# Performance work log

Measured on AMD Instinct MI355X. Metric: run time of the kernel, lower is better.

Reference implementation:

```python
import jax, jax.numpy as jnp
import numpy as np

D_MODEL = 1024
SCALE = 1.0 / np.sqrt(D_MODEL)


def setup_inputs() -> dict:
    key = jax.random.key(0)
    ks = jax.random.split(key, 9)
    B, S, D = 4, 2048, D_MODEL
    std = 1.0 / np.sqrt(D)
    x = jax.random.normal(ks[0], (B, S, D), dtype=jnp.float32)
    # nn.Linear weights: [out, in]; we store transposed [in, out] for x @ W
    Wq = jax.random.uniform(ks[1], (D, D), jnp.float32, -std, std)
    bq = jax.random.uniform(ks[2], (D,), jnp.float32, -std, std)
    Wk = jax.random.uniform(ks[3], (D, D), jnp.float32, -std, std)
    bk = jax.random.uniform(ks[4], (D,), jnp.float32, -std, std)
    Wv = jax.random.uniform(ks[5], (D, D), jnp.float32, -std, std)
    bv = jax.random.uniform(ks[6], (D,), jnp.float32, -std, std)
    Wo = jax.random.uniform(ks[7], (D, D), jnp.float32, -std, std)
    bo = jax.random.uniform(ks[8], (D,), jnp.float32, -std, std)
    return {"x": x, "Wq": Wq, "bq": bq, "Wk": Wk, "bk": bk,
            "Wv": Wv, "bv": bv, "Wo": Wo, "bo": bo}


def reference(x, Wq, bq, Wk, bk, Wv, bv, Wo, bo):
    q = x @ Wq + bq                      # [B,S,D]
    k = x @ Wk + bk
    v = x @ Wv + bv
    scores = jnp.einsum('bsd,btd->bst', q, k) * SCALE  # [B,S,S]
    weights = jax.nn.softmax(scores, axis=-1)
    out = jnp.einsum('bst,btd->bsd', weights, v)       # [B,S,D]
    return out @ Wo + bo
```

## Files before the change

### kernel.cpp

```cpp
#include <hip/hip_runtime.h>
#include <hip/hip_bf16.h>
#include <cstdint>

typedef __bf16 bf16x8 __attribute__((ext_vector_type(8)));
typedef float f32x4 __attribute__((ext_vector_type(4)));

__device__ __forceinline__ float bf2f(unsigned short u) {
  union { unsigned int i; float f; } x; x.i = ((unsigned int)u) << 16; return x.f;
}
__device__ __forceinline__ unsigned short f2bf(float f) {
  __hip_bfloat16 h = __float2bfloat16(f);
  return __builtin_bit_cast(unsigned short, h);
}

__device__ __forceinline__ void gload_lds16(const void* g, void* l) {
  auto gp = reinterpret_cast<__attribute__((address_space(1))) char*>(
      reinterpret_cast<uintptr_t>(g));
  auto lp = reinterpret_cast<__attribute__((address_space(3))) char*>(
      reinterpret_cast<uintptr_t>(l));
  __builtin_amdgcn_global_load_lds(gp, lp, 16, 0, 0);
}

__device__ __forceinline__ void xcd_swz(int& bx, int& by, int& bz) {
  const int gx = gridDim.x, gy = gridDim.y;
  const int n = gx * gy * (int)gridDim.z;
  int lin = blockIdx.x + gx * (blockIdx.y + gy * blockIdx.z);
  lin = (lin & 7) * (n >> 3) + (lin >> 3);
  bx = lin % gx; lin /= gx;
  by = lin % gy; bz = lin / gy;
}

__global__ __launch_bounds__(256) void cvt_f32_to_bf16(
    const float* __restrict__ in, unsigned short* __restrict__ out, long n4) {
  long i = (long)blockIdx.x * 256 + threadIdx.x;
  if (i >= n4) return;
  const float4 v = reinterpret_cast<const float4*>(in)[i];
  ushort4 o;
  o.x = f2bf(v.x); o.y = f2bf(v.y); o.z = f2bf(v.z); o.w = f2bf(v.w);
  reinterpret_cast<ushort4*>(out)[i] = o;
}

__global__ void transpose_w4(const float* __restrict__ w0,
                             const float* __restrict__ w1,
                             const float* __restrict__ w2,
                             const float* __restrict__ w3,
                             const float* __restrict__ b0,
                             const float* __restrict__ b1,
                             const float* __restrict__ b2,
                             unsigned short* __restrict__ out,
                             float* __restrict__ bqkv) {
  const int z = blockIdx.z;
  const float* in = (z == 0) ? w0 : (z == 1) ? w1 : (z == 2) ? w2 : w3;
  out += (size_t)z * 1024 * 1024;
  if (z < 3 && blockIdx.x == 0 && blockIdx.y == 0) {
    const float* src = (z == 0) ? b0 : (z == 1) ? b1 : b2;
    const int i = threadIdx.y * 32 + threadIdx.x;
    bqkv[z * 1024 + i] = src[i];
  }
  __shared__ float tile[32][33];
  const int c0 = blockIdx.x * 32, r0 = blockIdx.y * 32;
  tile[threadIdx.y][threadIdx.x] =
      in[(size_t)(r0 + threadIdx.y) * 1024 + c0 + threadIdx.x];
  __syncthreads();
  out[(size_t)(c0 + threadIdx.y) * 1024 + r0 + threadIdx.x] =
      f2bf(tile[threadIdx.x][threadIdx.y]);
}

template <typename OutT, bool HAS_BIAS, bool VSPLIT, bool EXPOUT, bool DIVSUM>
__global__ __launch_bounds__(256, 4) void gemm_hi(
    const unsigned short* __restrict__ A,
    const unsigned short* __restrict__ Bt,
    OutT* __restrict__ C,
    const float* __restrict__ bias,
    unsigned short* __restrict__ vt,
    int K, int lda, int ldb, int ldc, float scale,
    long sA, long sB, long sC) {
  int bx, by, bz;
  xcd_swz(bx, by, bz);
  A  += (long)bz * sA;
  Bt += (long)bz * sB;
  C  += (long)bz * sC;
  if constexpr (DIVSUM) bias += (long)bz * 2048;
  const int n0 = bx << 7;
  const int m0 = by << 7;
  __shared__ __attribute__((aligned(16))) unsigned short As[128 * 64];
  __shared__ __attribute__((aligned(16))) unsigned short Bs[128 * 64];
  const int t = threadIdx.x;
  const int lane = t & 63;
  const int w = t >> 6;
  const int wm = w >> 1, wn = w & 1;
  const unsigned short* gA = A + (size_t)m0 * lda;
  const unsigned short* gB = Bt + (size_t)n0 * ldb;
  const int NT = K >> 6;

  const int srow = lane >> 3;
  const int scol = ((lane & 7) ^ srow) << 3;

  f32x4 acc[4][4];
  const f32x4 vz = {0.f, 0.f, 0.f, 0.f};
#pragma unroll
  for (int i = 0; i < 4; ++i)
#pragma unroll
    for (int j = 0; j < 4; ++j) acc[i][j] = vz;

  for (int kt = 0; kt < NT; ++kt) {
    const unsigned short* pA = gA + (size_t)kt * 64;
    const unsigned short* pB = gB + (size_t)kt * 64;
#pragma unroll
    for (int i = 0; i < 4; ++i) {
      const int r0 = (w << 3) + (i << 5);
      gload_lds16(pA + (size_t)(r0 + srow) * lda + scol, As + r0 * 64);
      gload_lds16(pB + (size_t)(r0 + srow) * ldb + scol, Bs + r0 * 64);
    }
    __syncthreads();

#pragma unroll
    for (int kk = 0; kk < 2; ++kk) {
      bf16x8 af[4], bg[4];
      const int ch = ((kk << 2) + (lane >> 4)) ^ (lane & 7);
#pragma unroll
      for (int m = 0; m < 4; ++m) {
        const int row = (wm << 6) + (m << 4) + (lane & 15);
        af[m] = *reinterpret_cast<const bf16x8*>(As + row * 64 + (ch << 3));
      }
#pragma unroll
      for (int n = 0; n < 4; ++n) {
        const int row = (wn << 6) + (n << 4) + (lane & 15);
        bg[n] = *reinterpret_cast<const bf16x8*>(Bs + row * 64 + (ch << 3));
      }
#pragma unroll
      for (int m = 0; m < 4; ++m)
#pragma unroll
        for (int n = 0; n < 4; ++n) {
          if constexpr (VSPLIT) {
            acc[m][n] = __builtin_amdgcn_mfma_f32_16x16x32_bf16(
                af[m], bg[n], acc[m][n], 0, 0, 0);
          } else {
            acc[m][n] = __builtin_amdgcn_mfma_f32_16x16x32_bf16(
                bg[n], af[m], acc[m][n], 0, 0, 0);
          }
        }
    }
    __syncthreads();
  }

  if constexpr (VSPLIT) {
    const int crow0 = m0 + (wm << 6) + ((lane >> 4) << 2);
    const int ccol0 = n0 + (wn << 6) + (lane & 15);
    if (n0 >= 2048) {
      const int b = m0 >> 11;
#pragma unroll
      for (int mf = 0; mf < 4; ++mf) {
#pragma unroll
        for (int nf = 0; nf < 4; ++nf) {
          const int col = ccol0 + (nf << 4);
          const float bb = HAS_BIAS ? bias[col] : 0.f;
          const int d = col - 2048;
          const int s = (crow0 & 2047) + (mf << 4);
          ushort4 o;
          o.x = f2bf(acc[mf][nf][0] * scale + bb);
          o.y = f2bf(acc[mf][nf][1] * scale + bb);
          o.z = f2bf(acc[mf][nf][2] * scale + bb);
          o.w = f2bf(acc[mf][nf][3] * scale + bb);
          *reinterpret_cast<ushort4*>(
              vt + (((size_t)b << 10) + d) * 2048 + s) = o;
        }
      }
    } else {
#pragma unroll
      for (int mf = 0; mf < 4; ++mf) {
#pragma unroll
        for (int nf = 0; nf < 4; ++nf) {
          const int col = ccol0 + (nf << 4);
          const float bb = HAS_BIAS ? bias[col] : 0.f;
#pragma unroll
          for (int i = 0; i < 4; ++i) {
            const int row = crow0 + (mf << 4) + i;
            C[(size_t)row * ldc + col] =
                (OutT)f2bf(acc[mf][nf][i] * scale + bb);
          }
        }
      }
    }
  } else {
    const int mrow0 = m0 + (wm << 6) + (lane & 15);
    const int ncol0 = n0 + (wn << 6) + ((lane >> 4) << 2);
#pragma unroll
    for (int mf = 0; mf < 4; ++mf) {
      const int row = mrow0 + (mf << 4);
      float inv = 1.f;
      if constexpr (DIVSUM) inv = 1.f / bias[row];
#pragma unroll
      for (int nf = 0; nf < 4; ++nf) {
        const int col = ncol0 + (nf << 4);
        const f32x4 a = acc[mf][nf];
        if constexpr (EXPOUT) {
          ushort4 o;
          o.x = f2bf(__expf(a[0] * scale));
          o.y = f2bf(__expf(a[1] * scale));
          o.z = f2bf(__expf(a[2] * scale));
          o.w = f2bf(__expf(a[3] * scale));
          *reinterpret_cast<ushort4*>(&C[(size_t)row * ldc + col]) = o;
        } else if constexpr (DIVSUM) {
          ushort4 o;
          o.x = f2bf(a[0] * inv);
          o.y = f2bf(a[1] * inv);
          o.z = f2bf(a[2] * inv);
          o.w = f2bf(a[3] * inv);
          *reinterpret_cast<ushort4*>(&C[(size_t)row * ldc + col]) = o;
        } else {
          float4 bb = {0.f, 0.f, 0.f, 0.f};
          if (HAS_BIAS) bb = *reinterpret_cast<const float4*>(bias + col);
          if constexpr (sizeof(OutT) == 2) {
            ushort4 o;
            o.x = f2bf(a[0] * scale + bb.x);
            o.y = f2bf(a[1] * scale + bb.y);
            o.z = f2bf(a[2] * scale + bb.z);
            o.w = f2bf(a[3] * scale + bb.w);
            *reinterpret_cast<ushort4*>(&C[(size_t)row * ldc + col]) = o;
          } else {
            float4 o;
            o.x = a[0] * scale + bb.x;
            o.y = a[1] * scale + bb.y;
            o.z = a[2] * scale + bb.z;
            o.w = a[3] * scale + bb.w;
            *reinterpret_cast<float4*>(&C[(size_t)row * ldc + col]) = o;
          }
        }
      }
    }
  }
}

__global__ __launch_bounds__(256) void rowsum_bf16(
    const unsigned short* __restrict__ P, float* __restrict__ sums, int S) {
  const size_t row = blockIdx.x;
  const unsigned short* p = P + row * (size_t)S;
  const int t = threadIdx.x;
  const int lane = t & 63, w = t >> 6;
  const uint4 raw = reinterpret_cast<const uint4*>(p)[t];
  unsigned int u[4] = {raw.x, raw.y, raw.z, raw.w};
  float s = 0.f;
#pragma unroll
  for (int j = 0; j < 4; ++j) {
    s += bf2f((unsigned short)(u[j] & 0xffffu));
    s += bf2f((unsigned short)(u[j] >> 16));
  }
#pragma unroll
  for (int off = 32; off >= 1; off >>= 1) s += __shfl_xor(s, off, 64);
  __shared__ float red[4];
  if (lane == 0) red[w] = s;
  __syncthreads();
  if (t == 0) sums[row] = red[0] + red[1] + red[2] + red[3];
}

extern "C" void kernel_launch(void* const* d_in, const int* in_sizes, int n_in,
                              void* d_out, int out_size, void* d_ws, size_t ws_size,
                              hipStream_t stream) {
  (void)in_sizes; (void)n_in; (void)out_size; (void)ws_size;
  const float* x  = (const float*)d_in[0];
  const float* Wq = (const float*)d_in[1];
  const float* bq = (const float*)d_in[2];
  const float* Wk = (const float*)d_in[3];
  const float* bk = (const float*)d_in[4];
  const float* Wv = (const float*)d_in[5];
  const float* bv = (const float*)d_in[6];
  const float* Wo = (const float*)d_in[7];
  const float* bo = (const float*)d_in[8];
  float* out = (float*)d_out;

  constexpr int B = 4, S = 2048, D = 1024;
  constexpr long BS = (long)B * S;
  constexpr size_t MB = 1ull << 20;
  char* ws = (char*)d_ws;
  unsigned short* xb   = (unsigned short*)(ws + 0);
  unsigned short* Wall = (unsigned short*)(ws + 16 * MB);
  float*          bqkv = (float*)(ws + 24 * MB);
  float*          rsum = (float*)(ws + 24 * MB + 65536);
  unsigned short* QKVc = (unsigned short*)(ws + 25 * MB);
  unsigned short* Vt   = (unsigned short*)(ws + 57 * MB);
  unsigned short* Sc   = (unsigned short*)(ws + 73 * MB);
  unsigned short* AO   = (unsigned short*)(ws + 0);

  const float scale = 0.03125f;

  cvt_f32_to_bf16<<<(BS * D / 4 + 255) / 256, 256, 0, stream>>>(x, xb, BS * D / 4);
  transpose_w4<<<dim3(32, 32, 4), dim3(32, 32), 0, stream>>>(
      Wq, Wk, Wv, Wo, bq, bk, bv, Wall, bqkv);

  gemm_hi<unsigned short, true, true, false, false>
      <<<dim3(24, 64, 1), 256, 0, stream>>>(
      xb, Wall, QKVc, bqkv, Vt, D, D, D, 2048, 1.f, 0, 0, 0);

  gemm_hi<unsigned short, false, false, true, false>
      <<<dim3(16, 16, 4), 256, 0, stream>>>(
      QKVc + 0, QKVc + 1024, Sc, nullptr, nullptr, D, 2048, 2048, S, scale,
      (long)S * 2048, (long)S * 2048, (long)S * S);

  rowsum_bf16<<<B * S, 256, 0, stream>>>(Sc, rsum, S);

  gemm_hi<unsigned short, false, false, false, true>
      <<<dim3(8, 16, 4), 256, 0, stream>>>(
      Sc, Vt, AO, rsum, nullptr, S, S, S, D, 1.f,
      (long)S * S, (long)D * S, (long)S * D);

  gemm_hi<float, true, false, false, false>
      <<<dim3(8, 64, 1), 256, 0, stream>>>(
      AO, Wall + 3 * 1024 * 1024, out, bo, nullptr, D, D, D, D, 1.f, 0, 0, 0);
}
```

Measured before the change: 199.7 us.

## Fuse softmax row sums into score GEMM epilogue and remap QKV blocks per XCD

The exp-score GEMM epilogue now writes per-tile partial row sums into a small buffer. The P·V GEMM reduces the 32 partials per row before dividing, which removes the separate rowsum kernel that re-read the whole bf16 score matrix. The QKV projection GEMM also gets a custom block-to-XCD mapping, so that blocks sharing the same A rows land on the same XCD for L2 reuse. The exchange is extra epilogue shuffles, plus sums taken from fp32 exps rather than from the bf16-rounded values.

```diff
diff --git a/kernel.cpp b/kernel.cpp
--- a/kernel.cpp
+++ b/kernel.cpp
@@ -66,21 +66,30 @@
       f2bf(tile[threadIdx.x][threadIdx.y]);
 }
 
-template <typename OutT, bool HAS_BIAS, bool VSPLIT, bool EXPOUT, bool DIVSUM>
+template <typename OutT, bool HAS_BIAS, bool VSPLIT, bool EXPOUT, bool DIVSUM,
+          bool ROWXCD>
 __global__ __launch_bounds__(256, 4) void gemm_hi(
     const unsigned short* __restrict__ A,
     const unsigned short* __restrict__ Bt,
     OutT* __restrict__ C,
     const float* __restrict__ bias,
     unsigned short* __restrict__ vt,
+    float* __restrict__ psum,
     int K, int lda, int ldb, int ldc, float scale,
     long sA, long sB, long sC) {
   int bx, by, bz;
-  xcd_swz(bx, by, bz);
+  if constexpr (ROWXCD) {
+    const int lin = blockIdx.x + 24 * blockIdx.y;
+    const int xcd = lin & 7, idx = lin >> 3;
+    by = xcd + ((idx / 24) << 3);
+    bx = idx % 24;
+    bz = 0;
+  } else {
+    xcd_swz(bx, by, bz);
+  }
   A  += (long)bz * sA;
   Bt += (long)bz * sB;
   C  += (long)bz * sC;
-  if constexpr (DIVSUM) bias += (long)bz * 2048;
   const int n0 = bx << 7;
   const int m0 = by << 7;
   __shared__ __attribute__((aligned(16))) unsigned short As[128 * 64];
@@ -189,17 +198,29 @@
     for (int mf = 0; mf < 4; ++mf) {
       const int row = mrow0 + (mf << 4);
       float inv = 1.f;
-      if constexpr (DIVSUM) inv = 1.f / bias[row];
+      if constexpr (DIVSUM) {
+        const float* pr = bias + ((long)bz * 2048 + row) * 32;
+        float s = 0.f;
+#pragma unroll
+        for (int q = 0; q < 8; ++q) {
+          const float4 sv = *reinterpret_cast<const float4*>(pr + q * 4);
+          s += (sv.x + sv.y) + (sv.z + sv.w);
+        }
+        inv = 1.f / s;
+      }
+      float ps = 0.f;
 #pragma unroll
       for (int nf = 0; nf < 4; ++nf) {
         const int col = ncol0 + (nf << 4);
         const f32x4 a = acc[mf][nf];
         if constexpr (EXPOUT) {
+          const float e0 = __expf(a[0] * scale);
+          const float e1 = __expf(a[1] * scale);
+          const float e2 = __expf(a[2] * scale);
+          const float e3 = __expf(a[3] * scale);
+          ps += (e0 + e1) + (e2 + e3);
           ushort4 o;
-          o.x = f2bf(__expf(a[0] * scale));
-          o.y = f2bf(__expf(a[1] * scale));
-          o.z = f2bf(__expf(a[2] * scale));
-          o.w = f2bf(__expf(a[3] * scale));
+          o.x = f2bf(e0); o.y = f2bf(e1); o.z = f2bf(e2); o.w = f2bf(e3);
           *reinterpret_cast<ushort4*>(&C[(size_t)row * ldc + col]) = o;
         } else if constexpr (DIVSUM) {
           ushort4 o;
@@ -228,30 +249,14 @@
           }
         }
       }
+      if constexpr (EXPOUT) {
+        ps += __shfl_xor(ps, 16, 64);
+        ps += __shfl_xor(ps, 32, 64);
+        if ((lane >> 4) == 0)
+          psum[((long)bz * 2048 + row) * 32 + (bx << 1) + wn] = ps;
+      }
     }
   }
-}
-
-__global__ __launch_bounds__(256) void rowsum_bf16(
-    const unsigned short* __restrict__ P, float* __restrict__ sums, int S) {
-  const size_t row = blockIdx.x;
-  const unsigned short* p = P + row * (size_t)S;
-  const int t = threadIdx.x;
-  const int lane = t & 63, w = t >> 6;
-  const uint4 raw = reinterpret_cast<const uint4*>(p)[t];
-  unsigned int u[4] = {raw.x, raw.y, raw.z, raw.w};
-  float s = 0.f;
-#pragma unroll
-  for (int j = 0; j < 4; ++j) {
-    s += bf2f((unsigned short)(u[j] & 0xffffu));
-    s += bf2f((unsigned short)(u[j] >> 16));
-  }
-#pragma unroll
-  for (int off = 32; off >= 1; off >>= 1) s += __shfl_xor(s, off, 64);
-  __shared__ float red[4];
-  if (lane == 0) red[w] = s;
-  __syncthreads();
-  if (t == 0) sums[row] = red[0] + red[1] + red[2] + red[3];
 }
 
 extern "C" void kernel_launch(void* const* d_in, const int* in_sizes, int n_in,
@@ -276,10 +281,10 @@
   unsigned short* xb   = (unsigned short*)(ws + 0);
   unsigned short* Wall = (unsigned short*)(ws + 16 * MB);
   float*          bqkv = (float*)(ws + 24 * MB);
-  float*          rsum = (float*)(ws + 24 * MB + 65536);
-  unsigned short* QKVc = (unsigned short*)(ws + 25 * MB);
-  unsigned short* Vt   = (unsigned short*)(ws + 57 * MB);
-  unsigned short* Sc   = (unsigned short*)(ws + 73 * MB);
+  float*          psum = (float*)(ws + 24 * MB + 65536);
+  unsigned short* QKVc = (unsigned short*)(ws + 26 * MB);
+  unsigned short* Vt   = (unsigned short*)(ws + 58 * MB);
+  unsigned short* Sc   = (unsigned short*)(ws + 74 * MB);
   unsigned short* AO   = (unsigned short*)(ws + 0);
 
   const float scale = 0.03125f;
@@ -288,23 +293,22 @@
   transpose_w4<<<dim3(32, 32, 4), dim3(32, 32), 0, stream>>>(
       Wq, Wk, Wv, Wo, bq, bk, bv, Wall, bqkv);
 
-  gemm_hi<unsigned short, true, true, false, false>
+  gemm_hi<unsigned short, true, true, false, false, true>
       <<<dim3(24, 64, 1), 256, 0, stream>>>(
-      xb, Wall, QKVc, bqkv, Vt, D, D, D, 2048, 1.f, 0, 0, 0);
-
-  gemm_hi<unsigned short, false, false, true, false>
+      xb, Wall, QKVc, bqkv, Vt, nullptr, D, D, D, 2048, 1.f, 0, 0, 0);
+
+  gemm_hi<unsigned short, false, false, true, false, false>
       <<<dim3(16, 16, 4), 256, 0, stream>>>(
-      QKVc + 0, QKVc + 1024, Sc, nullptr, nullptr, D, 2048, 2048, S, scale,
-      (long)S * 2048, (long)S * 2048, (long)S * S);
-
-  rowsum_bf16<<<B * S, 256, 0, stream>>>(Sc, rsum, S);
-
-  gemm_hi<unsigned short, false, false, false, true>
+      QKVc + 0, QKVc + 1024, Sc, nullptr, nullptr, psum, D, 2048, 2048, S,
+      scale, (long)S * 2048, (long)S * 2048, (long)S * S);
+
+  gemm_hi<unsigned short, false, false, false, true, false>
       <<<dim3(8, 16, 4), 256, 0, stream>>>(
-      Sc, Vt, AO, rsum, nullptr, S, S, S, D, 1.f,
+      Sc, Vt, AO, psum, nullptr, nullptr, S, S, S, D, 1.f,
       (long)S * S, (long)D * S, (long)S * D);
 
-  gemm_hi<float, true, false, false, false>
+  gemm_hi<float, true, false, false, false, false>
       <<<dim3(8, 64, 1), 256, 0, stream>>>(
-      AO, Wall + 3 * 1024 * 1024, out, bo, nullptr, D, D, D, D, 1.f, 0, 0, 0);
-}
+      AO, Wall + 3 * 1024 * 1024, out, bo, nullptr, nullptr, D, D, D, D, 1.f,
+      0, 0, 0);
+}
```

Result: no change. 199.0 us, median of 2 (-0.4%).
